# Kernel optimization log

Hardware: AMD Instinct MI355X
Metric: run time of the kernel (lower is better)

The kernel has to match this reference:

```python
import jax, jax.numpy as jnp
import numpy as np

SEARCH_RANGE = 4  # max displacement -> 9x9 = 81 offsets
LEAKY_ALPHA = 0.1


def setup_inputs() -> dict:
    key = jax.random.key(0)
    k1, k2, k3 = jax.random.split(key, 3)
    B, H, W, C = 16, 96, 96, 128
    prv = jax.random.normal(k1, (B, H, W, C), dtype=jnp.float32)
    nxt = jax.random.normal(k2, (B, H, W, C), dtype=jnp.float32)
    # Conv2D(filters=2, kernel_size=3, padding='same'); in_channels = 81 + 2*C = 337
    fan_in, fan_out = 3 * 3 * 337, 3 * 3 * 2
    limit = np.sqrt(6.0 / (fan_in + fan_out))  # glorot_uniform
    conv_w = jax.random.uniform(k3, (3, 3, 337, 2), minval=-limit, maxval=limit, dtype=jnp.float32)
    conv_b = jnp.zeros((2,), dtype=jnp.float32)
    return {"prv": prv, "nxt": nxt, "conv_w": conv_w, "conv_b": conv_b}


def _cost_volume(prv, nxt):
    sr = SEARCH_RANGE
    padded = jnp.pad(nxt, ((0, 0), (sr, sr), (sr, sr), (0, 0)))
    H, W = prv.shape[1], prv.shape[2]
    n = 2 * sr + 1
    # 81 fixed static offsets: slice + per-pixel channel-mean correlation
    costs = [
        jnp.mean(prv * jax.lax.slice(padded, (0, y, x, 0), (padded.shape[0], y + H, x + W, padded.shape[3])), axis=-1)
        for y in range(n) for x in range(n)
    ]
    cost = jnp.stack(costs, axis=-1)  # [B, H, W, 81]
    return jnp.where(cost >= 0, cost, LEAKY_ALPHA * cost)  # leaky_relu(0.1)


def reference(prv, nxt, conv_w, conv_b):
    cost = _cost_volume(prv, nxt)
    feat = jnp.concatenate([cost, prv, nxt], axis=-1)  # [B, H, W, 337]
    out = jax.lax.conv_general_dilated(
        feat, conv_w, window_strides=(1, 1), padding='SAME',
        dimension_numbers=('NHWC', 'HWIO', 'NHWC'))
    return out + conv_b  # [B, H, W, 2]
```

## Files before the change

### kernel.cpp

```cpp
#include <hip/hip_runtime.h>
#include <hip/hip_fp16.h>

#define HH 96
#define WW 96
#define CC 128

#define RS 25
#define PS 17

typedef float f32x4 __attribute__((ext_vector_type(4)));
typedef short short8 __attribute__((ext_vector_type(8)));
typedef _Float16 f16x8 __attribute__((ext_vector_type(8)));

union U32H2 { unsigned int u; __half2 h; };
__device__ __forceinline__ unsigned int pack2(float x, float y){ U32H2 t; t.h=__floats2half2_rn(x,y); return t.u; }

__device__ __forceinline__ unsigned short f2bf(float x){
  unsigned int u = __float_as_uint(x);
  return (unsigned short)((u + 0x7FFFu + ((u >> 16) & 1u)) >> 16);
}
__device__ __forceinline__ unsigned int pkbf(float a, float b){
  return (unsigned)f2bf(a) | ((unsigned)f2bf(b) << 16);
}

union U4S8 { uint4 q; short8 s; };
union U4H8 { uint4 q; f16x8 h; };

template<int DY0, int NDY>
static __device__ __forceinline__ void cost_mma(const uint4* __restrict__ nt,
                                                int yr, int lq, int lm,
                                                short8 a, f32x4 (&acc)[5][2]) {
#pragma unroll
  for (int d = 0; d < NDY; ++d) {
    const int sb = ((yr + DY0 + d)*4 + lq)*RS;
    U4S8 b0, b1;
    b0.q = nt[sb + lm];
    b1.q = nt[sb + 16 + lm];
    acc[d][0] = __builtin_amdgcn_mfma_f32_16x16x32_bf16(a, b0.s, acc[d][0], 0, 0, 0);
    acc[d][1] = __builtin_amdgcn_mfma_f32_16x16x32_bf16(a, b1.s, acc[d][1], 0, 0, 0);
  }
}

__global__ __launch_bounds__(512, 4) void k_cost_mfma(const float* __restrict__ prv,
                                                      const float* __restrict__ nxt,
                                                      __half* __restrict__ cost) {
  const int x0 = blockIdx.x * 16;
  const int y0 = blockIdx.y * 4;
  const int b  = blockIdx.z;
  const int tid = threadIdx.x;
  const int w = tid >> 6, l = tid & 63;
  const int lm = l & 15, lq = l >> 4;
  const int yr = w >> 1, hf = w & 1;
  const int y = y0 + yr;

  __shared__ uint4 ntile[2][1232];
  __shared__ uint4 ptile[2][272];

  f32x4 acc[5][2];
#pragma unroll
  for (int d = 0; d < 5; ++d) {
    acc[d][0] = (f32x4){0.f,0.f,0.f,0.f};
    acc[d][1] = (f32x4){0.f,0.f,0.f,0.f};
  }

  const int p_px = tid >> 3, p_ch8 = tid & 7;
  const int p_row = p_px >> 4, p_col = p_px & 15;
  const float* prow = &prv[((size_t)(b*HH + y0 + p_row)*WW + x0 + p_col)*CC + p_ch8*4];
  const int p_slot = (p_row*4 + (p_ch8 >> 1))*PS + p_col;
  const int p_half = p_ch8 & 1;

  auto stage = [&](int ks, int buf){
#pragma unroll
    for (int j = 0; j < 5; ++j) {
      const int s = j*512 + tid;
      if (s < 2304) {
        const int px = s >> 3, ch8 = s & 7;
        const int row = px / 24, col = px - 24*row;
        const int gr = y0 - 4 + row, gc = x0 - 4 + col;
        float4 f = make_float4(0.f,0.f,0.f,0.f);
        if ((unsigned)gr < HH && (unsigned)gc < WW)
          f = *(const float4*)&nxt[((size_t)(b*HH + gr)*WW + gc)*CC + ks*32 + ch8*4];
        uint2 d; d.x = pkbf(f.x, f.y); d.y = pkbf(f.z, f.w);
        *(uint2*)((unsigned int*)&ntile[buf][(row*4 + (ch8 >> 1))*RS + col] + (ch8 & 1)*2) = d;
      }
    }
    {
      const float4 f = *(const float4*)(prow + ks*32);
      uint2 d; d.x = pkbf(f.x, f.y); d.y = pkbf(f.z, f.w);
      *(uint2*)((unsigned int*)&ptile[buf][p_slot] + p_half*2) = d;
    }
  };

  stage(0, 0);

#pragma unroll 1
  for (int ks = 0; ks < 4; ++ks) {
    __syncthreads();
    if (ks < 3) stage(ks + 1, (ks + 1) & 1);

    const int cur = ks & 1;
    U4S8 af;
    af.q = ptile[cur][(yr*4 + lq)*PS + lm];
    const uint4* nt = ntile[cur];
    if (hf == 0) cost_mma<0,5>(nt, yr, lq, lm, af.s, acc);
    else         cost_mma<5,4>(nt, yr, lq, lm, af.s, acc);
  }

  const int DY0 = hf ? 5 : 0, NDY = hf ? 4 : 5;
#pragma unroll
  for (int t = 0; t < 2; ++t) {
#pragma unroll
    for (int reg = 0; reg < 4; ++reg) {
      const int m  = lq*4 + reg;
      const int od = t*16 + lm - m;
      if (od >= 0 && od <= 8) {
        __half* bp = &cost[((size_t)(b*HH + y)*WW + x0 + m)*96 + DY0*9 + od];
#pragma unroll
        for (int d = 0; d < 5; ++d) {
          if (d < NDY) {
            float v = acc[d][t][reg] * 0.0078125f;
            v = (v >= 0.f) ? v : 0.1f * v;
            bp[d*9] = __float2half(v);
          }
        }
      }
    }
  }
}

__global__ __launch_bounds__(512) void k_conv_gemm(const float* __restrict__ prv,
                                                   const float* __restrict__ nxt,
                                                   const __half* __restrict__ cost,
                                                   const float* __restrict__ cw,
                                                   const float* __restrict__ cb,
                                                   float* __restrict__ out) {
  const int tw0 = blockIdx.x*16, th0 = blockIdx.y*16, b = blockIdx.z;
  const int tid = threadIdx.x;
  const int w = tid >> 6, l = tid & 63;
  const int lm = l & 15, lq = l >> 4;

  __shared__ __align__(16) char smem[49408];
  uint4*        feat16 = (uint4*)smem;
  float*        Gf     = (float*)smem;
  float2*       Gf2    = (float2*)smem;
  uint4*        B2     = (uint4*)(smem + 26880);
  __half*       B2h    = (__half*)(smem + 26880);

#pragma unroll 1
  for (int i = tid; i < 5632; i += 512) ((unsigned int*)B2)[i] = 0u;
#pragma unroll 1
  for (int i = tid; i < 240; i += 512) ((unsigned int*)smem)[6480 + i] = 0u;
#pragma unroll 1
  for (int i = tid; i < 352*18; i += 512) {
    const int ci = i / 18, j = i - 18*ci;
    if (ci >= 81 && ci < 96) continue;
    const int wci = (ci < 81) ? ci : ci - 15;
    const int tap = j >> 1, n = j & 1;
    const float v = cw[(tap*337 + wci)*2 + n];
    const int kk = ci & 31;
    B2h[((((ci >> 5)*4 + (kk >> 3))*32) + j)*8 + (kk & 7)] = __float2half(v);
  }

  f32x4 acc[3][2];
#pragma unroll
  for (int i = 0; i < 3; ++i) { acc[i][0] = (f32x4){0,0,0,0}; acc[i][1] = (f32x4){0,0,0,0}; }

#pragma unroll 1
  for (int kc = 0; kc < 11; ++kc) {
    __syncthreads();
#pragma unroll 1
    for (int i = tid; i < 648; i += 512) {
      const int px = i >> 1, half = i & 1;
      const int hr = px / 18, hc = px - 18*hr;
      const int gr = th0 - 1 + hr, gc = tw0 - 1 + hc;
      uint4 d0 = make_uint4(0,0,0,0), d1 = make_uint4(0,0,0,0);
      if ((unsigned)gr < HH && (unsigned)gc < WW) {
        const size_t pixi = (size_t)(b*HH + gr)*WW + gc;
        if (kc < 3) {
          const uint4* cs = (const uint4*)&cost[pixi*96 + kc*32 + half*16];
          d0 = cs[0]; d1 = cs[1];
        } else {
          const float* src = (kc < 7) ? prv : nxt;
          const int c0 = ((kc < 7) ? (kc-3) : (kc-7))*32 + half*16;
          const float4 f0 = *(const float4*)&src[pixi*128 + c0];
          const float4 f1 = *(const float4*)&src[pixi*128 + c0 + 4];
          const float4 f2 = *(const float4*)&src[pixi*128 + c0 + 8];
          const float4 f3 = *(const float4*)&src[pixi*128 + c0 + 12];
          d0 = make_uint4(pack2(f0.x,f0.y), pack2(f0.z,f0.w), pack2(f1.x,f1.y), pack2(f1.z,f1.w));
          d1 = make_uint4(pack2(f2.x,f2.y), pack2(f2.z,f2.w), pack2(f3.x,f3.y), pack2(f3.z,f3.w));
        }
      }
      feat16[5*px + 2*half]     = d0;
      feat16[5*px + 2*half + 1] = d1;
    }
    __syncthreads();

    U4H8 bf0, bf1;
    bf0.q = B2[(kc*4 + lq)*32 + lm];
    bf1.q = B2[(kc*4 + lq)*32 + 16 + lm];
#pragma unroll
    for (int i = 0; i < 3; ++i) {
      const int mf = w + 8*i;
      if (mf < 21) {
        U4H8 af;
        af.q = feat16[5*(16*mf + lm) + lq];
        acc[i][0] = __builtin_amdgcn_mfma_f32_16x16x32_f16(af.h, bf0.h, acc[i][0], 0, 0, 0);
        acc[i][1] = __builtin_amdgcn_mfma_f32_16x16x32_f16(af.h, bf1.h, acc[i][1], 0, 0, 0);
      }
    }
  }
  __syncthreads();

#pragma unroll
  for (int i = 0; i < 3; ++i) {
    const int mf = w + 8*i;
    if (mf >= 21) continue;
#pragma unroll
    for (int r = 0; r < 4; ++r) {
      const int px = 16*mf + lq*4 + r;
      if (px < 324) {
        Gf[px*20 + lm] = acc[i][0][r];
        if (lm < 2) Gf[px*20 + 16 + lm] = acc[i][1][r];
      }
    }
  }
  __syncthreads();

  if (tid < 512) {
    const int px = tid >> 1, n = tid & 1;
    const int ty = px >> 4, tx = px & 15;
    float s = cb[n];
#pragma unroll
    for (int p = 0; p < 9; ++p) {
      const int dy = p / 3, dx = p - 3*dy;
      const int hp = (ty + dy)*18 + (tx + dx);
      const float2 g = Gf2[hp*10 + p];
      s += n ? g.y : g.x;
    }
    out[((size_t)(b*HH + th0 + ty)*WW + (tw0 + tx))*2 + n] = s;
  }
}

extern "C" void kernel_launch(void* const* d_in, const int* in_sizes, int n_in,
                              void* d_out, int out_size, void* d_ws, size_t ws_size,
                              hipStream_t stream) {
  const float* prv = (const float*)d_in[0];
  const float* nxt = (const float*)d_in[1];
  const float* cw  = (const float*)d_in[2];
  const float* cb  = (const float*)d_in[3];
  __half* cost = (__half*)d_ws;

  k_cost_mfma<<<dim3(6, 24, 16), dim3(512), 0, stream>>>(prv, nxt, cost);
  k_conv_gemm<<<dim3(6, 6, 16), dim3(512), 0, stream>>>(prv, nxt, cost, cw, cb, (float*)d_out);
}
```

Before: 115.7 us.

## Pre-convert inputs to fp16 once and feed both kernels half-precision data

Adds a conversion kernel that writes fp16 copies of prv and nxt to workspace. The cost-volume kernel then stages fp16 tiles directly and uses fp16 MFMA instead of bf16. The conv kernel loads the halves without per-load packing. This removes repeated fp32 reads and conversions, since nxt was read about 2.25x per tile with halo, in exchange for an extra write/read pass over 75MB of fp16 and one more launch. The occupancy hint on the cost kernel is also raised.

```diff
diff --git a/kernel.cpp b/kernel.cpp
--- a/kernel.cpp
+++ b/kernel.cpp
@@ -9,40 +9,44 @@
 #define PS 17
 
 typedef float f32x4 __attribute__((ext_vector_type(4)));
-typedef short short8 __attribute__((ext_vector_type(8)));
 typedef _Float16 f16x8 __attribute__((ext_vector_type(8)));
 
 union U32H2 { unsigned int u; __half2 h; };
 __device__ __forceinline__ unsigned int pack2(float x, float y){ U32H2 t; t.h=__floats2half2_rn(x,y); return t.u; }
 
-__device__ __forceinline__ unsigned short f2bf(float x){
-  unsigned int u = __float_as_uint(x);
-  return (unsigned short)((u + 0x7FFFu + ((u >> 16) & 1u)) >> 16);
-}
-__device__ __forceinline__ unsigned int pkbf(float a, float b){
-  return (unsigned)f2bf(a) | ((unsigned)f2bf(b) << 16);
-}
-
-union U4S8 { uint4 q; short8 s; };
 union U4H8 { uint4 q; f16x8 h; };
+
+__global__ __launch_bounds__(256) void k_convert(const float* __restrict__ prv,
+                                                 const float* __restrict__ nxt,
+                                                 uint2* __restrict__ prv_h,
+                                                 uint2* __restrict__ nxt_h) {
+  const float4* src = (const float4*)(blockIdx.z ? nxt : prv);
+  uint2* dst = blockIdx.z ? nxt_h : prv_h;
+  const int total = 16*HH*WW*CC/4;
+  for (int i = blockIdx.x*256 + threadIdx.x; i < total; i += gridDim.x*256) {
+    const float4 f = src[i];
+    uint2 d; d.x = pack2(f.x, f.y); d.y = pack2(f.z, f.w);
+    dst[i] = d;
+  }
+}
 
 template<int DY0, int NDY>
 static __device__ __forceinline__ void cost_mma(const uint4* __restrict__ nt,
                                                 int yr, int lq, int lm,
-                                                short8 a, f32x4 (&acc)[5][2]) {
+                                                f16x8 a, f32x4 (&acc)[5][2]) {
 #pragma unroll
   for (int d = 0; d < NDY; ++d) {
     const int sb = ((yr + DY0 + d)*4 + lq)*RS;
-    U4S8 b0, b1;
+    U4H8 b0, b1;
     b0.q = nt[sb + lm];
     b1.q = nt[sb + 16 + lm];
-    acc[d][0] = __builtin_amdgcn_mfma_f32_16x16x32_bf16(a, b0.s, acc[d][0], 0, 0, 0);
-    acc[d][1] = __builtin_amdgcn_mfma_f32_16x16x32_bf16(a, b1.s, acc[d][1], 0, 0, 0);
-  }
-}
-
-__global__ __launch_bounds__(512, 4) void k_cost_mfma(const float* __restrict__ prv,
-                                                      const float* __restrict__ nxt,
+    acc[d][0] = __builtin_amdgcn_mfma_f32_16x16x32_f16(a, b0.h, acc[d][0], 0, 0, 0);
+    acc[d][1] = __builtin_amdgcn_mfma_f32_16x16x32_f16(a, b1.h, acc[d][1], 0, 0, 0);
+  }
+}
+
+__global__ __launch_bounds__(512, 6) void k_cost_mfma(const uint4* __restrict__ prv_h,
+                                                      const uint4* __restrict__ nxt_h,
                                                       __half* __restrict__ cost) {
   const int x0 = blockIdx.x * 16;
   const int y0 = blockIdx.y * 4;
@@ -63,32 +67,25 @@
     acc[d][1] = (f32x4){0.f,0.f,0.f,0.f};
   }
 
-  const int p_px = tid >> 3, p_ch8 = tid & 7;
-  const int p_row = p_px >> 4, p_col = p_px & 15;
-  const float* prow = &prv[((size_t)(b*HH + y0 + p_row)*WW + x0 + p_col)*CC + p_ch8*4];
-  const int p_slot = (p_row*4 + (p_ch8 >> 1))*PS + p_col;
-  const int p_half = p_ch8 & 1;
+  const int p_row = tid >> 6, p_c4 = (tid >> 4) & 3, p_col = tid & 15;
+  const size_t p_base = ((size_t)(b*HH + y0 + p_row)*WW + x0 + p_col)*16;
 
   auto stage = [&](int ks, int buf){
 #pragma unroll
-    for (int j = 0; j < 5; ++j) {
+    for (int j = 0; j < 3; ++j) {
       const int s = j*512 + tid;
-      if (s < 2304) {
-        const int px = s >> 3, ch8 = s & 7;
+      if (s < 1152) {
+        const int px = s >> 2, c4 = s & 3;
         const int row = px / 24, col = px - 24*row;
         const int gr = y0 - 4 + row, gc = x0 - 4 + col;
-        float4 f = make_float4(0.f,0.f,0.f,0.f);
+        uint4 d = make_uint4(0u,0u,0u,0u);
         if ((unsigned)gr < HH && (unsigned)gc < WW)
-          f = *(const float4*)&nxt[((size_t)(b*HH + gr)*WW + gc)*CC + ks*32 + ch8*4];
-        uint2 d; d.x = pkbf(f.x, f.y); d.y = pkbf(f.z, f.w);
-        *(uint2*)((unsigned int*)&ntile[buf][(row*4 + (ch8 >> 1))*RS + col] + (ch8 & 1)*2) = d;
-      }
-    }
-    {
-      const float4 f = *(const float4*)(prow + ks*32);
-      uint2 d; d.x = pkbf(f.x, f.y); d.y = pkbf(f.z, f.w);
-      *(uint2*)((unsigned int*)&ptile[buf][p_slot] + p_half*2) = d;
-    }
+          d = nxt_h[((size_t)(b*HH + gr)*WW + gc)*16 + ks*4 + c4];
+        ntile[buf][(row*4 + c4)*RS + col] = d;
+      }
+    }
+    if (tid < 256)
+      ptile[buf][(p_row*4 + p_c4)*PS + p_col] = prv_h[p_base + ks*4 + p_c4];
   };
 
   stage(0, 0);
@@ -99,11 +96,11 @@
     if (ks < 3) stage(ks + 1, (ks + 1) & 1);
 
     const int cur = ks & 1;
-    U4S8 af;
+    U4H8 af;
     af.q = ptile[cur][(yr*4 + lq)*PS + lm];
     const uint4* nt = ntile[cur];
-    if (hf == 0) cost_mma<0,5>(nt, yr, lq, lm, af.s, acc);
-    else         cost_mma<5,4>(nt, yr, lq, lm, af.s, acc);
+    if (hf == 0) cost_mma<0,5>(nt, yr, lq, lm, af.h, acc);
+    else         cost_mma<5,4>(nt, yr, lq, lm, af.h, acc);
   }
 
   const int DY0 = hf ? 5 : 0, NDY = hf ? 4 : 5;
@@ -128,8 +125,8 @@
   }
 }
 
-__global__ __launch_bounds__(512) void k_conv_gemm(const float* __restrict__ prv,
-                                                   const float* __restrict__ nxt,
+__global__ __launch_bounds__(512) void k_conv_gemm(const __half* __restrict__ prv_h,
+                                                   const __half* __restrict__ nxt_h,
                                                    const __half* __restrict__ cost,
                                                    const float* __restrict__ cw,
                                                    const float* __restrict__ cb,
@@ -176,19 +173,12 @@
       uint4 d0 = make_uint4(0,0,0,0), d1 = make_uint4(0,0,0,0);
       if ((unsigned)gr < HH && (unsigned)gc < WW) {
         const size_t pixi = (size_t)(b*HH + gr)*WW + gc;
-        if (kc < 3) {
-          const uint4* cs = (const uint4*)&cost[pixi*96 + kc*32 + half*16];
-          d0 = cs[0]; d1 = cs[1];
-        } else {
-          const float* src = (kc < 7) ? prv : nxt;
-          const int c0 = ((kc < 7) ? (kc-3) : (kc-7))*32 + half*16;
-          const float4 f0 = *(const float4*)&src[pixi*128 + c0];
-          const float4 f1 = *(const float4*)&src[pixi*128 + c0 + 4];
-          const float4 f2 = *(const float4*)&src[pixi*128 + c0 + 8];
-          const float4 f3 = *(const float4*)&src[pixi*128 + c0 + 12];
-          d0 = make_uint4(pack2(f0.x,f0.y), pack2(f0.z,f0.w), pack2(f1.x,f1.y), pack2(f1.z,f1.w));
-          d1 = make_uint4(pack2(f2.x,f2.y), pack2(f2.z,f2.w), pack2(f3.x,f3.y), pack2(f3.z,f3.w));
-        }
+        const unsigned short* sp;
+        if (kc < 3)      sp = (const unsigned short*)cost  + pixi*96  + kc*32 + half*16;
+        else if (kc < 7) sp = (const unsigned short*)prv_h + pixi*128 + (kc-3)*32 + half*16;
+        else             sp = (const unsigned short*)nxt_h + pixi*128 + (kc-7)*32 + half*16;
+        const uint4* q = (const uint4*)sp;
+        d0 = q[0]; d1 = q[1];
       }
       feat16[5*px + 2*half]     = d0;
       feat16[5*px + 2*half + 1] = d1;
@@ -248,8 +238,13 @@
   const float* nxt = (const float*)d_in[1];
   const float* cw  = (const float*)d_in[2];
   const float* cb  = (const float*)d_in[3];
-  __half* cost = (__half*)d_ws;
-
-  k_cost_mfma<<<dim3(6, 24, 16), dim3(512), 0, stream>>>(prv, nxt, cost);
-  k_conv_gemm<<<dim3(6, 6, 16), dim3(512), 0, stream>>>(prv, nxt, cost, cw, cb, (float*)d_out);
-}
+
+  char* wsb = (char*)d_ws;
+  __half* cost  = (__half*)wsb;
+  __half* prv_h = (__half*)(wsb + 28311552);
+  __half* nxt_h = (__half*)(wsb + 28311552 + 37748736);
+
+  k_convert<<<dim3(1024, 1, 2), dim3(256), 0, stream>>>(prv, nxt, (uint2*)prv_h, (uint2*)nxt_h);
+  k_cost_mfma<<<dim3(6, 24, 16), dim3(512), 0, stream>>>((const uint4*)prv_h, (const uint4*)nxt_h, cost);
+  k_conv_gemm<<<dim3(6, 6, 16), dim3(512), 0, stream>>>(prv_h, nxt_h, cost, cw, cb, (float*)d_out);
+}
```

Result: slower. 118.9 us (+2.7%).
